# Optimization experiments

Hardware: AMD Instinct MI355X
Metric: run time of the kernel (lower is better)

The kernel has to match this reference:

```python
import jax, jax.numpy as jnp
import numpy as np

D_MODEL = 1024
N_HEADS = 16
D_K = D_MODEL // N_HEADS
EPS = 0.1  # module's self.epsilon default


def setup_inputs() -> dict:
    key = jax.random.key(0)
    ks = jax.random.split(key, 9)
    B, S = 2, 2048
    x = jax.random.normal(ks[0], (B, S, D_MODEL), dtype=jnp.float32)
    qkv_w = jax.random.normal(ks[1], (3 * D_MODEL, D_MODEL), dtype=jnp.float32) * (1.0 / np.sqrt(D_MODEL))
    qkv_b = jax.random.normal(ks[2], (3 * D_MODEL,), dtype=jnp.float32) * 0.02
    out_w = jax.random.normal(ks[3], (D_MODEL, D_MODEL), dtype=jnp.float32) * (1.0 / np.sqrt(D_MODEL))
    out_b = jax.random.normal(ks[4], (D_MODEL,), dtype=jnp.float32) * 0.02
    # anchors captured as per-(batch,head,channel) min/max over seq dim -> [B,H,1,d_k]
    base = jax.random.normal(ks[5], (B, N_HEADS, 1, D_K), dtype=jnp.float32)
    spread = jnp.abs(jax.random.normal(ks[6], (B, N_HEADS, 1, D_K), dtype=jnp.float32)) + 0.5
    anchor_k_min = base - spread
    anchor_k_max = base + spread
    base_v = jax.random.normal(ks[7], (B, N_HEADS, 1, D_K), dtype=jnp.float32)
    spread_v = jnp.abs(jax.random.normal(ks[8], (B, N_HEADS, 1, D_K), dtype=jnp.float32)) + 0.5
    anchor_v_min = base_v - spread_v
    anchor_v_max = base_v + spread_v
    return {"x": x, "qkv_w": qkv_w, "qkv_b": qkv_b, "out_w": out_w, "out_b": out_b,
            "anchor_k_min": anchor_k_min, "anchor_k_max": anchor_k_max,
            "anchor_v_min": anchor_v_min, "anchor_v_max": anchor_v_max}


def _guard_clamp(t, a_min, a_max):
    # valid interval = [max(t-eps, a_min), min(t+eps, a_max)], lo capped at hi, then clamp t
    lo = jnp.maximum(t - EPS, a_min)
    hi = jnp.minimum(t + EPS, a_max)
    lo = jnp.minimum(lo, hi)
    return jnp.maximum(lo, jnp.minimum(t, hi))


def reference(x, qkv_w, qkv_b, out_w, out_b,
              anchor_k_min, anchor_k_max, anchor_v_min, anchor_v_max):
    B, S, D = x.shape
    # fused QKV projection (torch Linear: y = x @ W^T + b)
    qkv = x @ qkv_w.T + qkv_b                               # [B,S,3D]
    qkv = qkv.reshape(B, S, 3, N_HEADS, D_K)
    qkv = jnp.transpose(qkv, (2, 0, 3, 1, 4))               # [3,B,H,S,dk]
    q, k, v = qkv[0], qkv[1], qkv[2]
    # guard mode: range-aware clamp of k and v against anchors
    k = _guard_clamp(k, anchor_k_min, anchor_k_max)
    v = _guard_clamp(v, anchor_v_min, anchor_v_max)
    scores = jnp.einsum('bhqd,bhkd->bhqk', q, k) / np.sqrt(D_K).astype(np.float32)
    attn = jax.nn.softmax(scores, axis=-1)
    out = jnp.einsum('bhqk,bhkd->bhqd', attn, v)            # [B,H,S,dk]
    out = jnp.transpose(out, (0, 2, 1, 3)).reshape(B, S, D)
    return out @ out_w.T + out_b
```

## Files before the change

kernel.cpp:

```cpp
#include <hip/hip_runtime.h>


typedef __bf16 bf16x8 __attribute__((ext_vector_type(8)));
typedef float f32x4 __attribute__((ext_vector_type(4)));

#define EPSG 0.1f
#define QSCALE 0.180336880f

__device__ __forceinline__ unsigned short f2bf(float f) {
  unsigned int u = __float_as_uint(f);
  u += 0x7FFFu + ((u >> 16) & 1u);
  return (unsigned short)(u >> 16);
}

__device__ __forceinline__ unsigned cvt_pk_bf16(float a, float b) {
  unsigned r;
  asm("v_cvt_pk_bf16_f32 %0, %1, %2" : "=v"(r) : "v"(a), "v"(b));
  return r;
}

__device__ __forceinline__ void gload_lds16(const void* g, void* l) {
  __builtin_amdgcn_global_load_lds(
      (const __attribute__((address_space(1))) void*)g,
      (__attribute__((address_space(3))) void*)l, 16, 0, 0);
}

__global__ __launch_bounds__(256) void cvt_f32_bf16(const float* __restrict__ in,
                                                    unsigned short* __restrict__ out,
                                                    int n4) {
  int i = blockIdx.x * 256 + threadIdx.x;
  if (i < n4) {
    float4 v = ((const float4*)in)[i];
    ushort4 o;
    o.x = f2bf(v.x); o.y = f2bf(v.y); o.z = f2bf(v.z); o.w = f2bf(v.w);
    ((ushort4*)out)[i] = o;
  }
}

__device__ __forceinline__ void stage128x64(const unsigned short* __restrict__ g,
                                            long ldb, long row0, long k0b,
                                            unsigned short* lds, int w, int l) {
  const char* gp = (const char*)g + (row0 + (long)(w * 8 + (l >> 3))) * ldb + k0b +
                   (long)(((l & 7) ^ (l >> 3)) << 4);
  char* lp = (char*)lds + w * 1024;
#pragma unroll
  for (int i = 0; i < 4; ++i) {
    gload_lds16(gp + (long)i * 32 * ldb, lp + i * 4096);
  }
}

__device__ __forceinline__ bf16x8 frag_ld(const unsigned short* lds, int row, int cb) {
  return *(const bf16x8*)((const char*)lds + row * 128 + (cb ^ ((row & 7) << 4)));
}

__device__ __forceinline__ void gemm_loop(const unsigned short* __restrict__ A,
                                          const unsigned short* __restrict__ Bm,
                                          long m0, long n0,
                                          unsigned short* aT, unsigned short* bT,
                                          int w, int l, f32x4 acc[4][4]) {
  const int wr = (w >> 1) * 64, wc = (w & 1) * 64;
  const int l15 = l & 15;
  for (int ks = 0; ks < 1024; ks += 64) {
    __syncthreads();
    stage128x64(A, 2048, m0, (long)ks * 2, aT, w, l);
    stage128x64(Bm, 2048, n0, (long)ks * 2, bT, w, l);
    __syncthreads();
#pragma unroll
    for (int kk = 0; kk < 2; ++kk) {
      const int cb = kk * 64 + (l >> 4) * 16;
      bf16x8 af[4], bfr[4];
#pragma unroll
      for (int t = 0; t < 4; ++t) af[t] = frag_ld(aT, wr + t * 16 + l15, cb);
#pragma unroll
      for (int t = 0; t < 4; ++t) bfr[t] = frag_ld(bT, wc + t * 16 + l15, cb);
#pragma unroll
      for (int mt = 0; mt < 4; ++mt)
#pragma unroll
        for (int nt = 0; nt < 4; ++nt)
          acc[mt][nt] = __builtin_amdgcn_mfma_f32_16x16x32_bf16(af[mt], bfr[nt],
                                                                acc[mt][nt], 0, 0, 0);
    }
  }
}

__global__ __launch_bounds__(256) void qkv_gemm(
    const unsigned short* __restrict__ xb, const unsigned short* __restrict__ wb,
    const float* __restrict__ bias,
    const float* __restrict__ akmin, const float* __restrict__ akmax,
    const float* __restrict__ avmin, const float* __restrict__ avmax,
    unsigned short* __restrict__ qo, unsigned short* __restrict__ ko,
    unsigned short* __restrict__ vto) {
  __shared__ __align__(16) unsigned short aT[128 * 64];
  __shared__ __align__(16) unsigned short bT[128 * 64];
  const int tid = threadIdx.x, l = tid & 63, w = tid >> 6;
  const long m0 = (long)blockIdx.y * 128, n0 = (long)blockIdx.x * 128;
  f32x4 acc[4][4] = {};
  gemm_loop(xb, wb, m0, n0, aT, bT, w, l, acc);

  const int wr = (w >> 1) * 64, wc = (w & 1) * 64;
  const int l15 = l & 15, lg = l >> 4;
  const int t = (int)(n0 >> 10);
#pragma unroll
  for (int nt = 0; nt < 4; ++nt) {
    const int n = (int)n0 + wc + nt * 16 + l15;
    const float bv = bias[n];
    const int h = (n >> 6) & 15, d = n & 63;
#pragma unroll
    for (int mt = 0; mt < 4; ++mt) {
      const long s0 = m0 + wr + mt * 16 + lg * 4;
      const int b = (int)(s0 >> 11), s_lo = (int)(s0 & 2047);
      const int bh = b * 16 + h;
      if (t == 0) {
#pragma unroll
        for (int j = 0; j < 4; ++j) {
          float v = (acc[mt][nt][j] + bv) * QSCALE;
          qo[((long)bh * 2048 + s_lo + j) * 64 + d] = f2bf(v);
        }
      } else if (t == 1) {
        const int ai = bh * 64 + d;
        const float amn = akmin[ai], amx = akmax[ai];
#pragma unroll
        for (int j = 0; j < 4; ++j) {
          float v = acc[mt][nt][j] + bv;
          float lo = fmaxf(v - EPSG, amn);
          float hi = fminf(v + EPSG, amx);
          lo = fminf(lo, hi);
          v = fmaxf(lo, fminf(v, hi));
          ko[((long)bh * 2048 + s_lo + j) * 64 + d] = f2bf(v);
        }
      } else {
        const int ai = bh * 64 + d;
        const float amn = avmin[ai], amx = avmax[ai];
        ushort4 pk;
        unsigned short* pp = (unsigned short*)&pk;
#pragma unroll
        for (int j = 0; j < 4; ++j) {
          float v = acc[mt][nt][j] + bv;
          float lo = fmaxf(v - EPSG, amn);
          float hi = fminf(v + EPSG, amx);
          lo = fminf(lo, hi);
          v = fmaxf(lo, fminf(v, hi));
          pp[j] = f2bf(v);
        }
        *(ushort4*)(vto + ((long)bh * 64 + d) * 2048 + s_lo) = pk;
      }
    }
  }
}

__global__ __launch_bounds__(256) void attn_fwd(
    const unsigned short* __restrict__ q, const unsigned short* __restrict__ k,
    const unsigned short* __restrict__ vt, unsigned short* __restrict__ o) {
  __shared__ __align__(16) unsigned short kT[2][64 * 64];
  __shared__ __align__(16) unsigned short vT[2][64 * 64];
  __shared__ __align__(16) unsigned short p_lds[4 * 16 * 64];
  const int tid = threadIdx.x, l = tid & 63, w = tid >> 6;
  const int l15 = l & 15, lg = l >> 4;
  const int qt = blockIdx.x, bh = blockIdx.y;

  const char* kbC = (const char*)(k + (long)bh * 2048 * 64);
  const char* vbC = (const char*)(vt + (long)bh * 64 * 2048);

  const unsigned short* qbase = q + ((long)bh * 2048 + qt * 64 + w * 16) * 64;
  bf16x8 qf[2];
#pragma unroll
  for (int kk = 0; kk < 2; ++kk)
    qf[kk] = *(const bf16x8*)(qbase + (long)l15 * 64 + kk * 32 + lg * 8);

  float m_run = -1e30f, l_part = 0.f;
  f32x4 oacc[4] = {};

  unsigned short* pw = p_lds + w * 1024;
  const int pswz = (l15 & 7) << 4;
  char* pwrow = (char*)pw + l15 * 128;
  const int srow = l >> 3;
  const int schk = ((l & 7) ^ srow) << 4;

#define STAGE_KV(kt_, buf_)                                                      \
  do {                                                                           \
    const char* sK = kbC + (long)((kt_)*64 + w * 8 + srow) * 128 + schk;         \
    char* dK = (char*)kT[buf_] + w * 1024;                                       \
    gload_lds16(sK, dK);                                                         \
    gload_lds16(sK + 32 * 128, dK + 4096);                                       \
    const char* sV = vbC + (long)(w * 8 + srow) * 4096 + (long)(kt_)*128 + schk; \
    char* dV = (char*)vT[buf_] + w * 1024;                                       \
    gload_lds16(sV, dV);                                                         \
    gload_lds16(sV + 32 * 4096, dV + 4096);                                      \
  } while (0)

  STAGE_KV(0, 0);
  asm volatile("s_waitcnt vmcnt(0)" ::: "memory");
  __syncthreads();

  for (int kt = 0; kt < 32; ++kt) {
    const int cur = kt & 1;
    if (kt < 31) STAGE_KV(kt + 1, cur ^ 1);
    const unsigned short* kTc = kT[cur];
    const unsigned short* vTc = vT[cur];

    f32x4 sc[4] = {};
    __builtin_amdgcn_s_setprio(1);
#pragma unroll
    for (int kk = 0; kk < 2; ++kk) {
      const int cb = kk * 64 + lg * 16;
#pragma unroll
      for (int ct = 0; ct < 4; ++ct) {
        const int row = ct * 16 + l15;
        bf16x8 kf = *(const bf16x8*)((const char*)kTc + row * 128 +
                                     (cb ^ ((row & 7) << 4)));
        sc[ct] = __builtin_amdgcn_mfma_f32_16x16x32_bf16(kf, qf[kk], sc[ct], 0, 0, 0);
      }
    }
    __builtin_amdgcn_s_setprio(0);

    float pm = fmaxf(fmaxf(fmaxf(sc[0][0], sc[0][1]), fmaxf(sc[0][2], sc[0][3])),
                     fmaxf(fmaxf(sc[1][0], sc[1][1]), fmaxf(sc[1][2], sc[1][3])));
    pm = fmaxf(pm,
               fmaxf(fmaxf(fmaxf(sc[2][0], sc[2][1]), fmaxf(sc[2][2], sc[2][3])),
                     fmaxf(fmaxf(sc[3][0], sc[3][1]), fmaxf(sc[3][2], sc[3][3]))));
    if (!__all(pm <= m_run + 11.5f)) {
      float mx = pm;
      mx = fmaxf(mx, __shfl_xor(mx, 16, 64));
      mx = fmaxf(mx, __shfl_xor(mx, 32, 64));
      mx = fmaxf(mx, m_run);
      const float alpha = __builtin_amdgcn_exp2f(m_run - mx);
      m_run = mx;
      l_part *= alpha;
#pragma unroll
      for (int dt = 0; dt < 4; ++dt) oacc[dt] *= alpha;
    }
    float rs = 0.f;
#pragma unroll
    for (int ct = 0; ct < 4; ++ct) {
      const float p0 = __builtin_amdgcn_exp2f(sc[ct][0] - m_run);
      const float p1 = __builtin_amdgcn_exp2f(sc[ct][1] - m_run);
      const float p2 = __builtin_amdgcn_exp2f(sc[ct][2] - m_run);
      const float p3 = __builtin_amdgcn_exp2f(sc[ct][3] - m_run);
      rs += (p0 + p1) + (p2 + p3);
      uint2 pk;
      pk.x = cvt_pk_bf16(p0, p1);
      pk.y = cvt_pk_bf16(p2, p3);
      *(uint2*)(pwrow + ((ct * 32 + lg * 8) ^ pswz)) = pk;
    }
    l_part += rs;

    __builtin_amdgcn_s_setprio(1);
#pragma unroll
    for (int kk = 0; kk < 2; ++kk) {
      const int cb = kk * 64 + lg * 16;
      bf16x8 pf = *(const bf16x8*)(pwrow + (cb ^ pswz));
#pragma unroll
      for (int dt = 0; dt < 4; ++dt) {
        const int row = dt * 16 + l15;
        bf16x8 vf = *(const bf16x8*)((const char*)vTc + row * 128 +
                                     (cb ^ ((row & 7) << 4)));
        oacc[dt] = __builtin_amdgcn_mfma_f32_16x16x32_bf16(vf, pf, oacc[dt], 0, 0, 0);
      }
    }
    __builtin_amdgcn_s_setprio(0);
    asm volatile("s_waitcnt vmcnt(0)" ::: "memory");
    __syncthreads();
  }

  float rs = l_part;
  rs += __shfl_xor(rs, 16, 64);
  rs += __shfl_xor(rs, 32, 64);
  const float inv = 1.f / rs;

  const int b = bh >> 4, h = bh & 15;
  const long s = (long)qt * 64 + w * 16 + l15;
  unsigned short* orow = o + ((long)b * 2048 + s) * 1024 + h * 64;
#pragma unroll
  for (int dt = 0; dt < 4; ++dt) {
    uint2 pk;
    pk.x = cvt_pk_bf16(oacc[dt][0] * inv, oacc[dt][1] * inv);
    pk.y = cvt_pk_bf16(oacc[dt][2] * inv, oacc[dt][3] * inv);
    *(uint2*)(orow + dt * 16 + lg * 4) = pk;
  }
#undef STAGE_KV
}

__global__ __launch_bounds__(256) void out_gemm(const unsigned short* __restrict__ ab,
                                                const unsigned short* __restrict__ wb,
                                                const float* __restrict__ bias,
                                                float* __restrict__ out) {
  __shared__ __align__(16) unsigned short aT[128 * 64];
  __shared__ __align__(16) unsigned short bT[128 * 64];
  const int tid = threadIdx.x, l = tid & 63, w = tid >> 6;
  const long m0 = (long)blockIdx.y * 128, n0 = (long)blockIdx.x * 128;
  f32x4 acc[4][4] = {};
  gemm_loop(ab, wb, m0, n0, aT, bT, w, l, acc);

  const int wr = (w >> 1) * 64, wc = (w & 1) * 64;
  const int l15 = l & 15, lg = l >> 4;
#pragma unroll
  for (int nt = 0; nt < 4; ++nt) {
    const int n = (int)n0 + wc + nt * 16 + l15;
    const float bv = bias[n];
#pragma unroll
    for (int mt = 0; mt < 4; ++mt) {
#pragma unroll
      for (int j = 0; j < 4; ++j) {
        const long m = m0 + wr + mt * 16 + lg * 4 + j;
        out[m * 1024 + n] = acc[mt][nt][j] + bv;
      }
    }
  }
}

extern "C" void kernel_launch(void* const* d_in, const int* in_sizes, int n_in,
                              void* d_out, int out_size, void* d_ws, size_t ws_size,
                              hipStream_t stream) {
  const float* x = (const float*)d_in[0];
  const float* qkv_w = (const float*)d_in[1];
  const float* qkv_b = (const float*)d_in[2];
  const float* out_w = (const float*)d_in[3];
  const float* out_b = (const float*)d_in[4];
  const float* akmin = (const float*)d_in[5];
  const float* akmax = (const float*)d_in[6];
  const float* avmin = (const float*)d_in[7];
  const float* avmax = (const float*)d_in[8];

  char* ws = (char*)d_ws;
  const long MB = 1024 * 1024;
  unsigned short* xb  = (unsigned short*)(ws + 0 * MB);
  unsigned short* wqb = (unsigned short*)(ws + 8 * MB);
  unsigned short* wob = (unsigned short*)(ws + 14 * MB);
  unsigned short* qb  = (unsigned short*)(ws + 16 * MB);
  unsigned short* kb  = (unsigned short*)(ws + 24 * MB);
  unsigned short* vtb = (unsigned short*)(ws + 32 * MB);
  unsigned short* ob  = (unsigned short*)(ws + 40 * MB);

  cvt_f32_bf16<<<4096, 256, 0, stream>>>(x, xb, 4096 * 1024 / 4);
  cvt_f32_bf16<<<3072, 256, 0, stream>>>(qkv_w, wqb, 3072 * 1024 / 4);
  cvt_f32_bf16<<<1024, 256, 0, stream>>>(out_w, wob, 1024 * 1024 / 4);
  qkv_gemm<<<dim3(24, 32), 256, 0, stream>>>(xb, wqb, qkv_b, akmin, akmax, avmin,
                                             avmax, qb, kb, vtb);
  attn_fwd<<<dim3(32, 32), 256, 0, stream>>>(qb, kb, vtb, ob);
  out_gemm<<<dim3(8, 32), 256, 0, stream>>>(ob, wob, out_b, (float*)d_out);
}
```

Baseline: 147.7 us.

## Load V fragments directly from global and remap blocks for XCD locality

Stops staging V tiles in LDS and loads each wave's V MFMA operands straight from global memory into registers every iteration. Also remaps the block index so all query tiles of a head run on the same XCD, aiming for better L2 reuse of K/V. This cuts LDS footprint and LDS reads, but makes each wave fetch V separately, with no prefetch distance, so memory latency may be exposed.

```diff
diff --git a/kernel.cpp b/kernel.cpp
--- a/kernel.cpp
+++ b/kernel.cpp
@@ -152,14 +152,17 @@
     const unsigned short* __restrict__ q, const unsigned short* __restrict__ k,
     const unsigned short* __restrict__ vt, unsigned short* __restrict__ o) {
   __shared__ __align__(16) unsigned short kT[2][64 * 64];
-  __shared__ __align__(16) unsigned short vT[2][64 * 64];
   __shared__ __align__(16) unsigned short p_lds[4 * 16 * 64];
   const int tid = threadIdx.x, l = tid & 63, w = tid >> 6;
   const int l15 = l & 15, lg = l >> 4;
-  const int qt = blockIdx.x, bh = blockIdx.y;
+
+  const int linear = blockIdx.y * 32 + blockIdx.x;
+  const int xcd = linear & 7, idx = linear >> 3;
+  const int bh = xcd * 4 + (idx >> 5);
+  const int qt = idx & 31;
 
   const char* kbC = (const char*)(k + (long)bh * 2048 * 64);
-  const char* vbC = (const char*)(vt + (long)bh * 64 * 2048);
+  const unsigned short* vbG = vt + (long)bh * 64 * 2048;
 
   const unsigned short* qbase = q + ((long)bh * 2048 + qt * 64 + w * 16) * 64;
   bf16x8 qf[2];
@@ -176,27 +179,29 @@
   const int srow = l >> 3;
   const int schk = ((l & 7) ^ srow) << 4;
 
-#define STAGE_KV(kt_, buf_)                                                      \
-  do {                                                                           \
-    const char* sK = kbC + (long)((kt_)*64 + w * 8 + srow) * 128 + schk;         \
-    char* dK = (char*)kT[buf_] + w * 1024;                                       \
-    gload_lds16(sK, dK);                                                         \
-    gload_lds16(sK + 32 * 128, dK + 4096);                                       \
-    const char* sV = vbC + (long)(w * 8 + srow) * 4096 + (long)(kt_)*128 + schk; \
-    char* dV = (char*)vT[buf_] + w * 1024;                                       \
-    gload_lds16(sV, dV);                                                         \
-    gload_lds16(sV + 32 * 4096, dV + 4096);                                      \
+#define STAGE_K(kt_, buf_)                                               \
+  do {                                                                   \
+    const char* sK = kbC + (long)((kt_)*64 + w * 8 + srow) * 128 + schk; \
+    char* dK = (char*)kT[buf_] + w * 1024;                               \
+    gload_lds16(sK, dK);                                                 \
+    gload_lds16(sK + 32 * 128, dK + 4096);                               \
   } while (0)
 
-  STAGE_KV(0, 0);
+  STAGE_K(0, 0);
   asm volatile("s_waitcnt vmcnt(0)" ::: "memory");
   __syncthreads();
 
   for (int kt = 0; kt < 32; ++kt) {
     const int cur = kt & 1;
-    if (kt < 31) STAGE_KV(kt + 1, cur ^ 1);
+    if (kt < 31) STAGE_K(kt + 1, cur ^ 1);
+    bf16x8 vfr[2][4];
+#pragma unroll
+    for (int kk = 0; kk < 2; ++kk)
+#pragma unroll
+      for (int dt = 0; dt < 4; ++dt)
+        vfr[kk][dt] = *(const bf16x8*)(vbG + (long)(dt * 16 + l15) * 2048 +
+                                       kt * 64 + kk * 32 + lg * 8);
     const unsigned short* kTc = kT[cur];
-    const unsigned short* vTc = vT[cur];
 
     f32x4 sc[4] = {};
     __builtin_amdgcn_s_setprio(1);
@@ -251,10 +256,8 @@
       bf16x8 pf = *(const bf16x8*)(pwrow + (cb ^ pswz));
 #pragma unroll
       for (int dt = 0; dt < 4; ++dt) {
-        const int row = dt * 16 + l15;
-        bf16x8 vf = *(const bf16x8*)((const char*)vTc + row * 128 +
-                                     (cb ^ ((row & 7) << 4)));
-        oacc[dt] = __builtin_amdgcn_mfma_f32_16x16x32_bf16(vf, pf, oacc[dt], 0, 0, 0);
+        oacc[dt] = __builtin_amdgcn_mfma_f32_16x16x32_bf16(vfr[kk][dt], pf,
+                                                           oacc[dt], 0, 0, 0);
       }
     }
     __builtin_amdgcn_s_setprio(0);
@@ -277,7 +280,7 @@
     pk.y = cvt_pk_bf16(oacc[dt][2] * inv, oacc[dt][3] * inv);
     *(uint2*)(orow + dt * 16 + lg * 4) = pk;
   }
-#undef STAGE_KV
+#undef STAGE_K
 }
 
 __global__ __launch_bounds__(256) void out_gemm(const unsigned short* __restrict__ ab,
```

New measurement: 256.3 us. +73.6%, slower.
